# Performance work log

Hardware: AMD Instinct MI355X
Metric: run time of the kernel (lower is better)

Reference implementation:

```python
import jax, jax.numpy as jnp
import numpy as np

GH, GW = 8, 8  # hypernetwork patch grid
EPS = 1e-5


def image_coords(b, h, w, dtype):
    # matches get_image_coordinates: channel0 = x (varies along W), channel1 = y (varies along H)
    xs = jnp.linspace(-1.0, 1.0, w, dtype=dtype)
    ys = jnp.linspace(-1.0, 1.0, h, dtype=dtype)
    X = jnp.broadcast_to(xs[None, :], (h, w))
    Y = jnp.broadcast_to(ys[:, None], (h, w))
    g = jnp.stack([X, Y], axis=0)  # [2,H,W]
    return jnp.broadcast_to(g[None], (b, 2, h, w))


def im2col3(x):
    # reflect-pad 3x3 im2col -> [B,C,9,H,W]
    H, W = x.shape[2], x.shape[3]
    xp = jnp.pad(x, ((0, 0), (0, 0), (1, 1), (1, 1)), mode='reflect')
    cols = [xp[:, :, i:i + H, j:j + W] for i in range(3) for j in range(3)]
    return jnp.stack(cols, axis=2)


def meta_dw3(x, wsig):
    # depthwise 3x3 conv with per-patch weights. wsig: [B, C*9, GH, GW]
    B, C, H, W = x.shape
    p, q = H // GH, W // GW
    cols = im2col3(x).reshape(B, C, 9, GH, p, GW, q)
    Wd = wsig.reshape(B, C, 9, GH, GW)
    out = jnp.einsum('bctuivj,bctuv->bcuivj', cols, Wd)
    return out.reshape(B, C, H, W)


def meta_pw(x, wsig, out_nc):
    # pointwise 1x1 conv with per-patch weights. wsig: [B, out_nc*C, GH, GW]
    B, C, H, W = x.shape
    p, q = H // GH, W // GW
    xr = x.reshape(B, C, GH, p, GW, q)
    Wp = wsig.reshape(B, out_nc, C, GH, GW)
    out = jnp.einsum('bcuivj,bocuv->bouivj', xr, Wp)
    return out.reshape(B, out_nc, H, W)


def batch_norm(x, g, b):
    m = jnp.mean(x, (0, 2, 3), keepdims=True)
    v = jnp.var(x, (0, 2, 3), keepdims=True)
    return (x - m) * jax.lax.rsqrt(v + EPS) * g[None, :, None, None] + b[None, :, None, None]


def relu6(x):
    return jnp.clip(x, 0.0, 6.0)


def hpir(x, wsig, out_nc, g_dw, b_dw, g_pw, b_pw):
    # HyperPatchInvertedResidual, expand_ratio=1, stride=1, in_nc != out_nc -> no residual
    C = x.shape[1]
    n_dw = C * 9
    h = relu6(batch_norm(meta_dw3(x, wsig[:, :n_dw]), g_dw, b_dw))
    h = batch_norm(meta_pw(h, wsig[:, n_dw:n_dw + out_nc * C], out_nc), g_pw, b_pw)
    return h


def resize_bilinear(p, hw):
    B, C = p.shape[0], p.shape[1]
    return jax.image.resize(p, (B, C, hw[0], hw[1]), method='bilinear')


def decoder_forward(x_img, f0, f1, w0, w1, w2,
                    g_dw0, b_dw0, g_pw0, b_pw0,
                    g_dw1, b_dw1, g_pw1, b_pw1,
                    g_dw2, b_dw2, g_pw2, b_pw2):
    feats = [x_img, f0, f1]  # [img] + features[:-1]
    level_w = [w0, w1, w2]
    level_out = [64, 32, 21]
    bn_p = [(g_dw0, b_dw0, g_pw0, b_pw0),
            (g_dw1, b_dw1, g_pw1, b_pw1),
            (g_dw2, b_dw2, g_pw2, b_pw2)]
    p = None
    for level in range(3):
        f = feats[-level - 1]
        if p is None:
            p = f
        else:
            if p.shape[2:] != f.shape[2:]:
                p = resize_bilinear(p, f.shape[2:])
            p = jnp.concatenate([f, p], axis=1)
        B, _, H, W = p.shape
        p = jnp.concatenate([image_coords(B, H, W, p.dtype), p], axis=1)
        g_dw, b_dw, g_pw, b_pw = bn_p[level]
        p = hpir(p, level_w[level], level_out[level], g_dw, b_dw, g_pw, b_pw)
    return p


def setup_inputs() -> dict:
    key = jax.random.key(0)
    ks = jax.random.split(key, 8)
    inp = {
        'x_img': jax.random.normal(ks[0], (4, 3, 256, 256), jnp.float32),
        'f0': jax.random.normal(ks[1], (4, 32, 64, 64), jnp.float32),
        'f1': jax.random.normal(ks[2], (4, 64, 32, 32), jnp.float32),
        'w0': jax.random.normal(ks[3], (4, 4818, 8, 8), jnp.float32) * 0.1,
        'w1': jax.random.normal(ks[4], (4, 4018, 8, 8), jnp.float32) * 0.1,
        'w2': jax.random.normal(ks[5], (4, 1110, 8, 8), jnp.float32) * 0.1,
    }
    for name, c in [('dw0', 66), ('pw0', 64), ('dw1', 98), ('pw1', 32), ('dw2', 37), ('pw2', 21)]:
        inp['g_' + name] = jnp.ones((c,), jnp.float32)
        inp['b_' + name] = jnp.zeros((c,), jnp.float32)
    return inp


def reference(x_img, f0, f1, w0, w1, w2,
              g_dw0, b_dw0, g_pw0, b_pw0,
              g_dw1, b_dw1, g_pw1, b_pw1,
              g_dw2, b_dw2, g_pw2, b_pw2):
    return decoder_forward(x_img, f0, f1, w0, w1, w2,
                           g_dw0, b_dw0, g_pw0, b_pw0,
                           g_dw1, b_dw1, g_pw1, b_pw1,
                           g_dw2, b_dw2, g_pw2, b_pw2)
```

## Files before the change

### kernel.cpp

```cpp
#include <hip/hip_runtime.h>

#define EPS 1e-5f

__device__ __forceinline__ int reflect_idx(int i, int n) {
    if (i < 0) return -i;
    if (i >= n) return 2 * n - 2 - i;
    return i;
}

__device__ __forceinline__ float bilin(const float* __restrict__ pb, int Hp, float sy, float sx) {
    int y0 = (int)floorf(sy), x0 = (int)floorf(sx);
    float fy = sy - y0, fx = sx - x0;
    int y0c = min(max(y0, 0), Hp - 1), y1c = min(max(y0 + 1, 0), Hp - 1);
    int x0c = min(max(x0, 0), Hp - 1), x1c = min(max(x0 + 1, 0), Hp - 1);
    float v00 = pb[y0c * Hp + x0c], v01 = pb[y0c * Hp + x1c];
    float v10 = pb[y1c * Hp + x0c], v11 = pb[y1c * Hp + x1c];
    return v00 * (1 - fy) * (1 - fx) + v01 * (1 - fy) * fx
         + v10 * fy * (1 - fx) + v11 * fy * fx;
}

__device__ __forceinline__ void reduce_ss_lds(const float* __restrict__ part,
                                              const float* __restrict__ g,
                                              const float* __restrict__ bb,
                                              float* ss, int C, float invN, int tid) {
    for (int c = tid; c < C; c += 256) {
        float s1 = 0.f, s2 = 0.f;
#pragma unroll 8
        for (int s = 0; s < 64; ++s) {
            s1 += part[s * 2 * C + 2 * c];
            s2 += part[s * 2 * C + 2 * c + 1];
        }
        float m = s1 * invN;
        float var = s2 * invN - m * m;
        float sc = g[c] * rsqrtf(var + EPS);
        ss[2 * c] = sc;
        ss[2 * c + 1] = bb[c] - m * sc;
    }
}

template <int LEVEL, bool WRITE>
__global__ __launch_bounds__(256)
void fused_dw_kernel(const float* __restrict__ feat, const float* __restrict__ prev,
                     const float* __restrict__ part_prev, const float* __restrict__ g_prev,
                     const float* __restrict__ b_prev, float invN_prev,
                     const float* __restrict__ wsig,
                     float* __restrict__ out, float* __restrict__ part) {
    constexpr int C    = LEVEL == 0 ? 66 : LEVEL == 1 ? 98 : 37;
    constexpr int H    = LEVEL == 0 ? 32 : LEVEL == 1 ? 64 : 256;
    constexpr int TILE = LEVEL == 2 ? 32 : 16;
    constexpr int NT   = H / TILE;
    constexpr int PXPT = (TILE * TILE) / 256;
    constexpr int WC   = LEVEL == 0 ? 4818 : LEVEL == 1 ? 4018 : 1110;
    constexpr int NF   = LEVEL == 0 ? 64 : LEVEL == 1 ? 32 : 3;
    constexpr int Hp   = LEVEL == 1 ? 32 : 64;
    constexpr int Cp   = LEVEL == 1 ? 64 : 32;
    constexpr int P    = H / 8;
    constexpr float SC = LEVEL == 1 ? 0.5f : 0.25f;
    constexpr int HS   = TILE + 2;
    constexpr int PSS  = (LEVEL == 0) ? 2 : 2 * Cp;

    __shared__ float sh[HS * HS];
    __shared__ float pssl[PSS];
    int tid = threadIdx.x, bid = blockIdx.x;
    int tile = bid % (NT * NT);
    int c = (bid / (NT * NT)) % C;
    int b = bid / (NT * NT * C);
    int ty0 = (tile / NT) * TILE, tx0 = (tile % NT) * TILE;

    if constexpr (LEVEL != 0) {
        reduce_ss_lds(part_prev, g_prev, b_prev, pssl, Cp, invN_prev, tid);
        __syncthreads();
    }

    for (int i = tid; i < HS * HS; i += 256) {
        int h = reflect_idx(ty0 - 1 + i / HS, H);
        int w = reflect_idx(tx0 - 1 + i % HS, H);
        float val;
        if (c == 0)      val = -1.f + 2.f * w / (H - 1);
        else if (c == 1) val = -1.f + 2.f * h / (H - 1);
        else if (c < 2 + NF) val = feat[((size_t)(b * NF + c - 2) * H + h) * H + w];
        else {
            int o = c - 2 - NF;
            const float* pb = prev + (size_t)(b * Cp + o) * Hp * Hp;
            float raw = bilin(pb, Hp, (h + 0.5f) * SC - 0.5f, (w + 0.5f) * SC - 0.5f);
            val = raw * pssl[2 * o] + pssl[2 * o + 1];
        }
        sh[i] = val;
    }
    __syncthreads();

    float s1 = 0.f, s2 = 0.f;
    float* ob = out + (((size_t)(b * C + c)) * H + ty0) * H + tx0;
    float wreg[9];
    if constexpr (TILE == P) {
        const float* wb = wsig + ((size_t)(b * WC + c * 9)) * 64 + (ty0 / P) * 8 + (tx0 / P);
#pragma unroll
        for (int t = 0; t < 9; ++t) wreg[t] = wb[(size_t)t * 64];
    }
#pragma unroll
    for (int k = 0; k < PXPT; ++k) {
        int px = tid + k * 256;
        int tyy = px / TILE, txx = px % TILE;
        if constexpr (TILE != P) {
            int u = (ty0 + tyy) / P, vv = (tx0 + txx) / P;
            const float* wb = wsig + ((size_t)(b * WC + c * 9)) * 64 + u * 8 + vv;
#pragma unroll
            for (int t = 0; t < 9; ++t) wreg[t] = wb[(size_t)t * 64];
        }
        float acc = 0.f;
#pragma unroll
        for (int t = 0; t < 9; ++t)
            acc += wreg[t] * sh[(tyy + t / 3) * HS + txx + t % 3];
        if constexpr (WRITE) ob[tyy * H + txx] = acc;
        s1 += acc; s2 += acc * acc;
    }
#pragma unroll
    for (int off = 32; off; off >>= 1) {
        s1 += __shfl_xor(s1, off);
        s2 += __shfl_xor(s2, off);
    }
    __shared__ float r1[4], r2[4];
    int wave = tid >> 6;
    if ((tid & 63) == 0) { r1[wave] = s1; r2[wave] = s2; }
    __syncthreads();
    if (tid == 0) {
        int slot = bid & 63;
        atomicAdd(&part[slot * 2 * C + 2 * c],     r1[0] + r1[1] + r1[2] + r1[3]);
        atomicAdd(&part[slot * 2 * C + 2 * c + 1], r2[0] + r2[1] + r2[2] + r2[3]);
    }
}

template <int C, int ONC, int H, int PX_T, int OC_T>
__global__ __launch_bounds__(256)
void pw_small_kernel(const float* __restrict__ x, const float* __restrict__ wsig,
                     const float* __restrict__ part_in, const float* __restrict__ g,
                     const float* __restrict__ bb, float invN,
                     float* __restrict__ out, float* __restrict__ part, int WC, int ndw) {
    constexpr int P = H / 8;
    constexpr int OC_I = ONC / OC_T;
    __shared__ float lw[ONC * C];
    __shared__ float lx[C * PX_T];
    __shared__ float ssl[2 * C];
    int tid = threadIdx.x, bid = blockIdx.x;
    int uv = bid & 63, b = bid >> 6;
    int u = uv >> 3, v = uv & 7;

    const size_t wbase = ((size_t)b * WC + ndw) * 64 + uv;
    for (int i = tid; i < ONC * C; i += 256) lw[i] = wsig[wbase + (size_t)i * 64];
    reduce_ss_lds(part_in, g, bb, ssl, C, invN, tid);
    __syncthreads();

    for (int i = tid; i < C * PX_T; i += 256) {
        int c = i / PX_T, pxl = i % PX_T;
        int h = u * P + pxl / P, w = v * P + pxl % P;
        float xv = x[(((size_t)b * C + c) * H + h) * H + w];
        lx[i] = fminf(fmaxf(xv * ssl[2 * c] + ssl[2 * c + 1], 0.f), 6.f);
    }
    __syncthreads();

    int px_id = tid % PX_T, oc_id = tid / PX_T;
    int h = u * P + px_id / P, w = v * P + px_id % P;
    float acc[OC_I];
#pragma unroll
    for (int oi = 0; oi < OC_I; ++oi) acc[oi] = 0.f;
    for (int c = 0; c < C; ++c) {
        float xv = lx[c * PX_T + px_id];
#pragma unroll
        for (int oi = 0; oi < OC_I; ++oi)
            acc[oi] += lw[(oc_id * OC_I + oi) * C + c] * xv;
    }
    float* ob = out + (((size_t)b * ONC) * H + h) * H + w;
#pragma unroll
    for (int oi = 0; oi < OC_I; ++oi)
        ob[(size_t)(oc_id * OC_I + oi) * H * H] = acc[oi];

    constexpr int GROUP = (PX_T < 64) ? PX_T : 64;
    int lane = tid & 63;
    int slot = bid & 63;
#pragma unroll
    for (int oi = 0; oi < OC_I; ++oi) {
        float s1 = acc[oi], s2 = acc[oi] * acc[oi];
#pragma unroll
        for (int off = GROUP / 2; off; off >>= 1) {
            s1 += __shfl_xor(s1, off);
            s2 += __shfl_xor(s2, off);
        }
        if ((lane & (GROUP - 1)) == 0) {
            int o = oc_id * OC_I + oi;
            atomicAdd(&part[slot * 2 * ONC + 2 * o], s1);
            atomicAdd(&part[slot * 2 * ONC + 2 * o + 1], s2);
        }
    }
}

__global__ __launch_bounds__(256)
void pw2_kernel(const float* __restrict__ x, const float* __restrict__ wsig,
                const float* __restrict__ part_in, const float* __restrict__ g,
                const float* __restrict__ bb,
                float* __restrict__ out, float* __restrict__ part) {
    const int C = 37, ONC = 21, H = 256, PATCH = 32, WC = 1110, NDW = 333;
    __shared__ float lw[ONC * C];
    __shared__ float ssl[2 * C];
    __shared__ float r1[4][ONC], r2[4][ONC];
    int tid = threadIdx.x, bid = blockIdx.x;
    int uv = bid & 63, b = bid >> 6;
    int y0 = (uv >> 3) * PATCH, x0 = (uv & 7) * PATCH;

    for (int i = tid; i < ONC * C; i += 256) lw[i] = wsig[((size_t)(b * WC + NDW) + i) * 64 + uv];
    reduce_ss_lds(part_in, g, bb, ssl, C, 1.f / 262144.f, tid);
    __syncthreads();

    int row = tid >> 3, col = (tid & 7) * 4;
    const float* xb = x + (((size_t)b * C) * H + y0 + row) * H + x0 + col;
    float4 acc[ONC];
#pragma unroll
    for (int o = 0; o < ONC; ++o) acc[o] = make_float4(0.f, 0.f, 0.f, 0.f);

    for (int c = 0; c < C; ++c) {
        float4 xv = *(const float4*)(xb + (size_t)c * H * H);
        float sc = ssl[2 * c], sb = ssl[2 * c + 1];
        xv.x = fminf(fmaxf(xv.x * sc + sb, 0.f), 6.f);
        xv.y = fminf(fmaxf(xv.y * sc + sb, 0.f), 6.f);
        xv.z = fminf(fmaxf(xv.z * sc + sb, 0.f), 6.f);
        xv.w = fminf(fmaxf(xv.w * sc + sb, 0.f), 6.f);
#pragma unroll
        for (int o = 0; o < ONC; ++o) {
            float wv = lw[o * C + c];
            acc[o].x += wv * xv.x;
            acc[o].y += wv * xv.y;
            acc[o].z += wv * xv.z;
            acc[o].w += wv * xv.w;
        }
    }
    float* ob = out + (((size_t)b * ONC) * H + y0 + row) * H + x0 + col;
#pragma unroll
    for (int o = 0; o < ONC; ++o) *(float4*)(ob + (size_t)o * H * H) = acc[o];

    int wave = tid >> 6, lane = tid & 63;
#pragma unroll
    for (int o = 0; o < ONC; ++o) {
        float s1 = acc[o].x + acc[o].y + acc[o].z + acc[o].w;
        float s2 = acc[o].x * acc[o].x + acc[o].y * acc[o].y
                 + acc[o].z * acc[o].z + acc[o].w * acc[o].w;
#pragma unroll
        for (int off = 32; off; off >>= 1) {
            s1 += __shfl_xor(s1, off);
            s2 += __shfl_xor(s2, off);
        }
        if (lane == 0) { r1[wave][o] = s1; r2[wave][o] = s2; }
    }
    __syncthreads();
    int slot = bid & 63;
    for (int o = tid; o < ONC; o += 256) {
        atomicAdd(&part[slot * 42 + 2 * o],     r1[0][o] + r1[1][o] + r1[2][o] + r1[3][o]);
        atomicAdd(&part[slot * 42 + 2 * o + 1], r2[0][o] + r2[1][o] + r2[2][o] + r2[3][o]);
    }
}

__global__ __launch_bounds__(256)
void finalbn_kernel(float* __restrict__ out, const float* __restrict__ part_in,
                    const float* __restrict__ g, const float* __restrict__ bb) {
    __shared__ float ssl[42];
    reduce_ss_lds(part_in, g, bb, ssl, 21, 1.f / 262144.f, threadIdx.x);
    __syncthreads();
    const int total4 = 4 * 21 * 256 * 256 / 4;
    for (int idx = blockIdx.x * 256 + threadIdx.x; idx < total4; idx += gridDim.x * 256) {
        int c = (idx / (256 * 256 / 4)) % 21;
        float4 v = ((float4*)out)[idx];
        float sc = ssl[2 * c], sb = ssl[2 * c + 1];
        v.x = v.x * sc + sb; v.y = v.y * sc + sb; v.z = v.z * sc + sb; v.w = v.w * sc + sb;
        ((float4*)out)[idx] = v;
    }
}

extern "C" void kernel_launch(void* const* d_in, const int* in_sizes, int n_in,
                              void* d_out, int out_size, void* d_ws, size_t ws_size,
                              hipStream_t stream) {
    const float* x_img = (const float*)d_in[0];
    const float* f0    = (const float*)d_in[1];
    const float* f1    = (const float*)d_in[2];
    const float* w0    = (const float*)d_in[3];
    const float* w1    = (const float*)d_in[4];
    const float* w2    = (const float*)d_in[5];
    const float* g_dw0 = (const float*)d_in[6],  *b_dw0 = (const float*)d_in[7];
    const float* g_pw0 = (const float*)d_in[8],  *b_pw0 = (const float*)d_in[9];
    const float* g_dw1 = (const float*)d_in[10], *b_dw1 = (const float*)d_in[11];
    const float* g_pw1 = (const float*)d_in[12], *b_pw1 = (const float*)d_in[13];
    const float* g_dw2 = (const float*)d_in[14], *b_dw2 = (const float*)d_in[15];
    const float* g_pw2 = (const float*)d_in[16], *b_pw2 = (const float*)d_in[17];
    float* out = (float*)d_out;
    float* ws = (float*)d_ws;

    float* part_dw0 = ws;
    float* part_pw0 = ws + 8448;
    float* part_dw1 = ws + 16640;
    float* part_pw1 = ws + 29184;
    float* part_dw2 = ws + 33280;
    float* part_pw2 = ws + 38016;
    float* pw0raw = ws + 40704;
    float* pw1raw = pw0raw + 262144;
    float* bigA   = pw1raw + 524288;

    hipMemsetAsync(ws, 0, 40704 * sizeof(float), stream);

    fused_dw_kernel<0, true><<<4 * 66 * 4, 256, 0, stream>>>(
        f1, nullptr, nullptr, nullptr, nullptr, 0.f, w0, bigA, part_dw0);
    pw_small_kernel<66, 64, 32, 16, 16><<<256, 256, 0, stream>>>(
        bigA, w0, part_dw0, g_dw0, b_dw0, 1.f / 4096.f, pw0raw, part_pw0, 4818, 594);
    fused_dw_kernel<1, true><<<4 * 98 * 16, 256, 0, stream>>>(
        f0, pw0raw, part_pw0, g_pw0, b_pw0, 1.f / 4096.f, w1, bigA, part_dw1);
    pw_small_kernel<98, 32, 64, 64, 4><<<256, 256, 0, stream>>>(
        bigA, w1, part_dw1, g_dw1, b_dw1, 1.f / 16384.f, pw1raw, part_pw1, 4018, 882);
    fused_dw_kernel<2, true><<<4 * 37 * 64, 256, 0, stream>>>(
        x_img, pw1raw, part_pw1, g_pw1, b_pw1, 1.f / 16384.f, w2, bigA, part_dw2);
    pw2_kernel<<<256, 256, 0, stream>>>(bigA, w2, part_dw2, g_dw2, b_dw2, out, part_pw2);
    finalbn_kernel<<<1024, 256, 0, stream>>>(out, part_pw2, g_pw2, b_pw2);
}
```

Baseline: 154.4 us.

## Add row-strip depthwise kernel for stage-2 with LDS halo tile and register blocking

Result: no change. 151.7 us (-1.7%).

```diff
diff --git a/kernel.cpp b/kernel.cpp
--- a/kernel.cpp
+++ b/kernel.cpp
@@ -130,6 +130,99 @@
     }
 }
 
+__global__ __launch_bounds__(256)
+void dw2_row_kernel(const float* __restrict__ ximg, const float* __restrict__ prev,
+                    const float* __restrict__ part_prev, const float* __restrict__ g_prev,
+                    const float* __restrict__ b_prev,
+                    const float* __restrict__ wsig,
+                    float* __restrict__ out, float* __restrict__ part) {
+    const int C = 37, H = 256, W = 256, WC = 1110, Hp = 64, Cp = 32;
+    const int S = 260;
+    __shared__ float sh[10 * S];
+    __shared__ float pssl[64];
+    __shared__ float lwv[72];
+    __shared__ float r1[4], r2[4];
+
+    int tid = threadIdx.x, bid = blockIdx.x;
+    int rb = bid & 31;
+    int c  = (bid >> 5) % C;
+    int b  = bid / (32 * C);
+    int ty0 = rb * 8;
+    int u = ty0 >> 5;
+
+    reduce_ss_lds(part_prev, g_prev, b_prev, pssl, Cp, 1.f / 16384.f, tid);
+    if (tid < 72) {
+        int v = tid / 9, t = tid % 9;
+        lwv[tid] = wsig[((size_t)(b * WC + c * 9 + t)) * 64 + u * 8 + v];
+    }
+    __syncthreads();
+
+    for (int i = tid; i < 10 * 258; i += 256) {
+        int r = i / 258, wcol = i % 258 - 1;
+        int h = reflect_idx(ty0 - 1 + r, H);
+        int w = reflect_idx(wcol, W);
+        float val;
+        if (c == 0)      val = -1.f + 2.f * w / 255.f;
+        else if (c == 1) val = -1.f + 2.f * h / 255.f;
+        else if (c < 5)  val = ximg[((size_t)(b * 3 + c - 2) * H + h) * W + w];
+        else {
+            int o = c - 5;
+            const float* pb = prev + (size_t)(b * Cp + o) * Hp * Hp;
+            float raw = bilin(pb, Hp, (h + 0.5f) * 0.25f - 0.5f, (w + 0.5f) * 0.25f - 0.5f);
+            val = raw * pssl[2 * o] + pssl[2 * o + 1];
+        }
+        sh[r * S + wcol + 1] = val;
+    }
+    __syncthreads();
+
+    int row = tid >> 5;
+    int col0 = (tid & 31) * 8;
+    int v = col0 >> 5;
+    float wr[9];
+#pragma unroll
+    for (int t = 0; t < 9; ++t) wr[t] = lwv[v * 9 + t];
+
+    float px[8];
+#pragma unroll
+    for (int k = 0; k < 8; ++k) px[k] = 0.f;
+
+#pragma unroll
+    for (int dr = 0; dr < 3; ++dr) {
+        const float* base = &sh[(row + dr) * S + col0];
+        float t0[10];
+        float4 q0 = *(const float4*)(base);
+        float4 q1 = *(const float4*)(base + 4);
+        t0[0] = q0.x; t0[1] = q0.y; t0[2] = q0.z; t0[3] = q0.w;
+        t0[4] = q1.x; t0[5] = q1.y; t0[6] = q1.z; t0[7] = q1.w;
+        t0[8] = base[8]; t0[9] = base[9];
+        float w0 = wr[dr * 3], w1 = wr[dr * 3 + 1], w2 = wr[dr * 3 + 2];
+#pragma unroll
+        for (int k = 0; k < 8; ++k)
+            px[k] += w0 * t0[k] + w1 * t0[k + 1] + w2 * t0[k + 2];
+    }
+
+    float* ob = out + (((size_t)(b * C + c)) * H + ty0 + row) * W + col0;
+    *(float4*)ob       = make_float4(px[0], px[1], px[2], px[3]);
+    *(float4*)(ob + 4) = make_float4(px[4], px[5], px[6], px[7]);
+
+    float s1 = 0.f, s2 = 0.f;
+#pragma unroll
+    for (int k = 0; k < 8; ++k) { s1 += px[k]; s2 += px[k] * px[k]; }
+#pragma unroll
+    for (int off = 32; off; off >>= 1) {
+        s1 += __shfl_xor(s1, off);
+        s2 += __shfl_xor(s2, off);
+    }
+    int wave = tid >> 6;
+    if ((tid & 63) == 0) { r1[wave] = s1; r2[wave] = s2; }
+    __syncthreads();
+    if (tid == 0) {
+        int slot = bid & 63;
+        atomicAdd(&part[slot * 2 * C + 2 * c],     r1[0] + r1[1] + r1[2] + r1[3]);
+        atomicAdd(&part[slot * 2 * C + 2 * c + 1], r2[0] + r2[1] + r2[2] + r2[3]);
+    }
+}
+
 template <int C, int ONC, int H, int PX_T, int OC_T>
 __global__ __launch_bounds__(256)
 void pw_small_kernel(const float* __restrict__ x, const float* __restrict__ wsig,
@@ -311,8 +404,8 @@
         f0, pw0raw, part_pw0, g_pw0, b_pw0, 1.f / 4096.f, w1, bigA, part_dw1);
     pw_small_kernel<98, 32, 64, 64, 4><<<256, 256, 0, stream>>>(
         bigA, w1, part_dw1, g_dw1, b_dw1, 1.f / 16384.f, pw1raw, part_pw1, 4018, 882);
-    fused_dw_kernel<2, true><<<4 * 37 * 64, 256, 0, stream>>>(
-        x_img, pw1raw, part_pw1, g_pw1, b_pw1, 1.f / 16384.f, w2, bigA, part_dw2);
+    dw2_row_kernel<<<4 * 37 * 32, 256, 0, stream>>>(
+        x_img, pw1raw, part_pw1, g_pw1, b_pw1, w2, bigA, part_dw2);
     pw2_kernel<<<256, 256, 0, stream>>>(bigA, w2, part_dw2, g_dw2, b_dw2, out, part_pw2);
     finalbn_kernel<<<1024, 256, 0, stream>>>(out, part_pw2, g_pw2, b_pw2);
 }
```
